# Kernel optimization log

Measured on AMD Instinct MI355X. Metric: run time of the kernel, lower is better.

## Reference

```python
import jax, jax.numpy as jnp
import numpy as np

B, IN, H = 4096, 1024, 2048

def setup_inputs() -> dict:
    key = jax.random.key(0)
    ks = jax.random.split(key, 7)
    sk = (1.0 / H) ** 0.5
    return {
        "x": jax.random.normal(ks[0], (B, IN), dtype=jnp.float32),
        "prev_h": jax.random.normal(ks[1], (B, H), dtype=jnp.float32),
        "prev_c": jax.random.normal(ks[2], (B, H), dtype=jnp.float32),
        "W_i": jax.random.uniform(ks[3], (H, H + IN), dtype=jnp.float32, minval=-sk, maxval=sk),
        "W_f": jax.random.uniform(ks[4], (H, H + IN), dtype=jnp.float32, minval=-sk, maxval=sk),
        "W_o": jax.random.uniform(ks[5], (H, H + IN), dtype=jnp.float32, minval=-sk, maxval=sk),
        "W_c": jax.random.uniform(ks[6], (H, H + IN), dtype=jnp.float32, minval=-sk, maxval=sk),
    }

def reference(x, prev_h, prev_c, W_i, W_f, W_o, W_c):
    # concat (h, x) along features: [B, H+IN]
    hx = jnp.concatenate([prev_h, x], axis=1)
    # stack 4 gate weights -> single GEMM: [B, H+IN] @ [H+IN, 4H]
    W = jnp.concatenate([W_i, W_f, W_o, W_c], axis=0)  # [4H, H+IN]
    gates = hx @ W.T  # [B, 4H]
    gi, gf, go, gc = jnp.split(gates, 4, axis=1)
    i = jax.nn.sigmoid(gi)
    f = jax.nn.sigmoid(gf)
    o = jax.nn.sigmoid(go)
    c_tilde = jnp.tanh(gc)
    next_c = f * prev_c + i * c_tilde
    next_h = o * jnp.tanh(next_c)
    return next_h, next_c
```

## Files before the change

kernel.cpp:

```cpp
#include <hip/hip_runtime.h>
#include <hip/hip_bf16.h>


#define BATCH 4096
#define INW   1024
#define HID   2048
#define GK    3072
#define GN    8192

typedef __attribute__((ext_vector_type(8))) short short8;
typedef __attribute__((ext_vector_type(4))) float floatx4;

__device__ __forceinline__ unsigned short f2bf(float f) {
    union { float f; unsigned u; } v; v.f = f;
    unsigned r = v.u + 0x7FFFu + ((v.u >> 16) & 1u);
    return (unsigned short)(r >> 16);
}
__device__ __forceinline__ float sigf(float x) {
    return 1.0f / (1.0f + __expf(-x));
}
__device__ __forceinline__ float tanhfast(float x) {
    float t = __expf(fminf(fmaxf(2.0f * x, -30.0f), 30.0f));
    return (t - 1.0f) / (t + 1.0f);
}

__global__ __launch_bounds__(256) void pack_all(const float4* __restrict__ ph,
                                                const float4* __restrict__ x,
                                                const float4* __restrict__ Wi,
                                                const float4* __restrict__ Wf,
                                                const float4* __restrict__ Wo,
                                                const float4* __restrict__ Wc,
                                                unsigned short* __restrict__ hx,
                                                unsigned short* __restrict__ Wb) {
    long i = (long)blockIdx.x * 256 + threadIdx.x;
    const float4* src;
    unsigned short* dst;
    if (i < 1048576L) {
        int r  = (int)(i >> 8);
        int c8 = (int)(i & 255);
        src = ph + 2 * i;
        dst = hx + (size_t)r * GK + (size_t)c8 * 8;
    } else if (i < 1572864L) {
        long j = i - 1048576L;
        int r  = (int)(j >> 7);
        int c8 = (int)(j & 127);
        src = x + 2 * j;
        dst = hx + (size_t)r * GK + HID + (size_t)c8 * 8;
    } else {
        long j = i - 1572864L;
        const float4* Wg;
        int g;
        if (j < 786432L)            { Wg = Wi; g = 0; }
        else if (j < 1572864L)      { Wg = Wf; g = 1; j -= 786432L; }
        else if (j < 2359296L)      { Wg = Wo; g = 2; j -= 1572864L; }
        else                        { Wg = Wc; g = 3; j -= 2359296L; }
        src = Wg + 2 * j;
        int h  = (int)(j / 384);
        int kc = (int)(j - (long)h * 384);
        dst = Wb + (size_t)(4 * h + g) * GK + (size_t)kc * 8;
    }
    float4 v0 = src[0];
    float4 v1 = src[1];
    unsigned short o[8];
    o[0] = f2bf(v0.x); o[1] = f2bf(v0.y); o[2] = f2bf(v0.z); o[3] = f2bf(v0.w);
    o[4] = f2bf(v1.x); o[5] = f2bf(v1.y); o[6] = f2bf(v1.z); o[7] = f2bf(v1.w);
    *(short8*)dst = *(const short8*)o;
}

__device__ __forceinline__ void gld16(const unsigned short* g, unsigned short* l) {
    __builtin_amdgcn_global_load_lds((const __attribute__((address_space(1))) unsigned int*)g,
                                     (__attribute__((address_space(3))) unsigned int*)l,
                                     16, 0, 0);
}

template<int VM> __device__ __forceinline__ void wait_vm() {
    if constexpr (VM == 8)      asm volatile("s_waitcnt vmcnt(8)" ::: "memory");
    else if constexpr (VM == 4) asm volatile("s_waitcnt vmcnt(4)" ::: "memory");
    else if constexpr (VM == 0) asm volatile("s_waitcnt vmcnt(0)" ::: "memory");
}

__global__ __launch_bounds__(512, 2) void gemm_fused(const unsigned short* __restrict__ A,
                                                     const unsigned short* __restrict__ Bt,
                                                     const float* __restrict__ prev_c,
                                                     float* __restrict__ out) {
    __shared__ unsigned short lds[65536];
    const int tid  = threadIdx.x;
    const int wave = tid >> 6;
    const int lane = tid & 63;

    const int bid = blockIdx.x;
    const int x = bid & 7, ii = bid >> 3;
    const int mt = ((x & 3) << 2) + (ii & 3);
    const int nt = ((x >> 2) << 4) + (ii >> 2);
    const long row0 = (long)mt * 256;
    const long col0 = (long)nt * 256;

    const int wm = wave >> 2;
    const int wn = wave & 3;

    const int c0 = ((tid & 3) - ((tid >> 3) & 3)) & 3;
    const unsigned short* gA0 = A  + (row0 + (tid >> 2)) * GK + c0 * 8;
    const unsigned short* gB0 = Bt + (col0 + (tid >> 2)) * GK + c0 * 8;

#define STAGE_A(kt, b) do { \
        unsigned short* _d = &lds[(b) * 8192 + tid * 8]; \
        gld16(gA0 + (size_t)(kt) * 32, _d); \
        gld16(gA0 + 128 * GK + (size_t)(kt) * 32, _d + 4096); \
    } while (0)
#define STAGE_B(kt, b) do { \
        unsigned short* _d = &lds[32768 + (b) * 8192 + tid * 8]; \
        gld16(gB0 + (size_t)(kt) * 32, _d); \
        gld16(gB0 + 128 * GK + (size_t)(kt) * 32, _d + 4096); \
    } while (0)

    const int fr = lane & 15;
    const int cq = lane >> 4;
    const int slot = ((cq + (fr >> 1)) & 3) << 3;
    const int aoff = (wm * 128 + fr) * 32 + slot;
    const int boff = (wn * 64 + fr) * 32 + slot;

    floatx4 acc[8][4];
    #pragma unroll
    for (int i = 0; i < 8; i++)
        #pragma unroll
        for (int j = 0; j < 4; j++)
            acc[i][j] = (floatx4)(0.0f);

    STAGE_A(0, 0); STAGE_B(0, 0);
    STAGE_A(1, 1); STAGE_B(1, 1);
    STAGE_A(2, 2); STAGE_B(2, 2);
    asm volatile("s_waitcnt vmcnt(8)" ::: "memory");
    __builtin_amdgcn_s_barrier();

#define K_ITER(t, VMW, STG) do { \
        const unsigned short* bufA = &lds[((t) & 3) * 8192]; \
        const unsigned short* bufB = &lds[32768 + ((t) & 3) * 8192]; \
        short8 af[4], af2[4], bfv[4]; \
        _Pragma("unroll") \
        for (int i = 0; i < 4; i++) af[i]  = *(const short8*)&bufA[aoff + i * 512]; \
        _Pragma("unroll") \
        for (int j = 0; j < 4; j++) bfv[j] = *(const short8*)&bufB[boff + j * 512]; \
        __builtin_amdgcn_sched_barrier(0);  \
        _Pragma("unroll") \
        for (int i = 0; i < 4; i++) af2[i] = *(const short8*)&bufA[aoff + 2048 + i * 512]; \
        if (STG) { STAGE_A((t) + 3, ((t) + 3) & 3); STAGE_B((t) + 3, ((t) + 3) & 3); } \
        asm volatile("s_waitcnt lgkmcnt(4)" ::: "memory"); \
        __builtin_amdgcn_sched_barrier(0); \
        __builtin_amdgcn_s_setprio(1); \
        _Pragma("unroll") \
        for (int i = 0; i < 4; i++) \
            _Pragma("unroll") \
            for (int j = 0; j < 4; j++) \
                acc[i][j] = __builtin_amdgcn_mfma_f32_16x16x32_bf16(af[i], bfv[j], acc[i][j], 0, 0, 0); \
        __builtin_amdgcn_s_setprio(0); \
        asm volatile("s_waitcnt lgkmcnt(0)" ::: "memory"); \
        __builtin_amdgcn_sched_barrier(0); \
        wait_vm<VMW>(); \
        __builtin_amdgcn_s_barrier(); \
        __builtin_amdgcn_sched_barrier(0); \
        __builtin_amdgcn_s_setprio(1); \
        _Pragma("unroll") \
        for (int i = 0; i < 4; i++) \
            _Pragma("unroll") \
            for (int j = 0; j < 4; j++) \
                acc[4 + i][j] = __builtin_amdgcn_mfma_f32_16x16x32_bf16(af2[i], bfv[j], acc[4 + i][j], 0, 0, 0); \
        __builtin_amdgcn_s_setprio(0); \
    } while (0)

    int t = 0;
    for (; t < 93; ++t) K_ITER(t, 8, true);
    K_ITER(93, 4, false);
    K_ITER(94, 0, false);
    K_ITER(95, -1, false);

#undef K_ITER
#undef STAGE_A
#undef STAGE_B

    const int cr = (lane >> 4) << 2;
    const int cc = lane & 15;
    const long hbase = col0 >> 2;
    float* gbuf = (float*)lds;

    #pragma unroll 1
    for (int pass = 0; pass < 2; ++pass) {
        __syncthreads();
        if (wm == pass) {
            #pragma unroll
            for (int mi = 0; mi < 8; mi++) {
                #pragma unroll
                for (int nj = 0; nj < 4; nj++) {
                    const int colb = wn * 64 + nj * 16 + cc;
                    #pragma unroll
                    for (int r = 0; r < 4; r++)
                        gbuf[(mi * 16 + cr + r) * 256 + colb] = acc[mi][nj][r];
                }
            }
        }
        __syncthreads();
        #pragma unroll 4
        for (int p = 0; p < 16; p++) {
            const int u   = p * 512 + tid;
            const int row = u >> 6;
            const int h   = u & 63;
            float4 g4 = *(const float4*)&gbuf[row * 256 + h * 4];
            const long grow = row0 + pass * 128 + row;
            const long ob   = grow * (long)HID + hbase + h;
            float pc = prev_c[ob];
            float iv = sigf(g4.x);
            float fv = sigf(g4.y);
            float ov = sigf(g4.z);
            float cv = tanhfast(g4.w);
            float nc = fv * pc + iv * cv;
            float nh = ov * tanhfast(nc);
            out[ob] = nh;
            out[(size_t)BATCH * HID + ob] = nc;
        }
    }
}

extern "C" void kernel_launch(void* const* d_in, const int* in_sizes, int n_in,
                              void* d_out, int out_size, void* d_ws, size_t ws_size,
                              hipStream_t stream) {
    const float* x   = (const float*)d_in[0];
    const float* ph  = (const float*)d_in[1];
    const float* pc  = (const float*)d_in[2];
    const float* Wi  = (const float*)d_in[3];
    const float* Wf  = (const float*)d_in[4];
    const float* Wo  = (const float*)d_in[5];
    const float* Wc  = (const float*)d_in[6];

    unsigned short* hx = (unsigned short*)d_ws;
    unsigned short* Wb = hx + (size_t)BATCH * GK;
    float* out = (float*)d_out;

    pack_all<<<18432, 256, 0, stream>>>((const float4*)ph, (const float4*)x,
                                        (const float4*)Wi, (const float4*)Wf,
                                        (const float4*)Wo, (const float4*)Wc,
                                        hx, Wb);

    gemm_fused<<<512, 512, 0, stream>>>(hx, Wb, pc, out);
}
```

Baseline: 402.2 us.

## Switch GEMM inner loop to 32x32x16 bf16 MFMA tiles

```diff
diff --git a/kernel.cpp b/kernel.cpp
--- a/kernel.cpp
+++ b/kernel.cpp
@@ -10,6 +10,7 @@
 
 typedef __attribute__((ext_vector_type(8))) short short8;
 typedef __attribute__((ext_vector_type(4))) float floatx4;
+typedef __attribute__((ext_vector_type(16))) float floatx16;
 
 __device__ __forceinline__ unsigned short f2bf(float f) {
     union { float f; unsigned u; } v; v.f = f;
@@ -113,18 +114,23 @@
         gld16(gB0 + 128 * GK + (size_t)(kt) * 32, _d + 4096); \
     } while (0)
 
-    const int fr = lane & 15;
-    const int cq = lane >> 4;
-    const int slot = ((cq + (fr >> 1)) & 3) << 3;
-    const int aoff = (wm * 128 + fr) * 32 + slot;
-    const int boff = (wn * 64 + fr) * 32 + slot;
-
-    floatx4 acc[8][4];
+    const int fr32 = lane & 31;
+    const int hk   = lane >> 5;
+    const int RA0  = wm * 128 + fr32;
+    const int RB0  = wn * 64 + fr32;
+    const int sA   = (RA0 >> 1) & 3;
+    const int sB   = (RB0 >> 1) & 3;
+    const int a_k0 = RA0 * 32 + (((hk)     + sA) & 3) * 8;
+    const int a_k1 = RA0 * 32 + (((2 + hk) + sA) & 3) * 8;
+    const int b_k0 = RB0 * 32 + (((hk)     + sB) & 3) * 8;
+    const int b_k1 = RB0 * 32 + (((2 + hk) + sB) & 3) * 8;
+
+    floatx16 acc[4][2];
     #pragma unroll
-    for (int i = 0; i < 8; i++)
+    for (int i = 0; i < 4; i++)
         #pragma unroll
-        for (int j = 0; j < 4; j++)
-            acc[i][j] = (floatx4)(0.0f);
+        for (int j = 0; j < 2; j++)
+            acc[i][j] = (floatx16)(0.0f);
 
     STAGE_A(0, 0); STAGE_B(0, 0);
     STAGE_A(1, 1); STAGE_B(1, 1);
@@ -135,36 +141,35 @@
 #define K_ITER(t, VMW, STG) do { \
         const unsigned short* bufA = &lds[((t) & 3) * 8192]; \
         const unsigned short* bufB = &lds[32768 + ((t) & 3) * 8192]; \
-        short8 af[4], af2[4], bfv[4]; \
-        _Pragma("unroll") \
-        for (int i = 0; i < 4; i++) af[i]  = *(const short8*)&bufA[aoff + i * 512]; \
-        _Pragma("unroll") \
-        for (int j = 0; j < 4; j++) bfv[j] = *(const short8*)&bufB[boff + j * 512]; \
-        __builtin_amdgcn_sched_barrier(0);  \
-        _Pragma("unroll") \
-        for (int i = 0; i < 4; i++) af2[i] = *(const short8*)&bufA[aoff + 2048 + i * 512]; \
+        short8 af0[4], af1[4], bf0[2], bf1[2]; \
+        _Pragma("unroll") \
+        for (int i = 0; i < 4; i++) { \
+            af0[i] = *(const short8*)&bufA[a_k0 + i * 1024]; \
+            af1[i] = *(const short8*)&bufA[a_k1 + i * 1024]; \
+        } \
+        _Pragma("unroll") \
+        for (int j = 0; j < 2; j++) { \
+            bf0[j] = *(const short8*)&bufB[b_k0 + j * 1024]; \
+            bf1[j] = *(const short8*)&bufB[b_k1 + j * 1024]; \
+        } \
         if (STG) { STAGE_A((t) + 3, ((t) + 3) & 3); STAGE_B((t) + 3, ((t) + 3) & 3); } \
-        asm volatile("s_waitcnt lgkmcnt(4)" ::: "memory"); \
+        __builtin_amdgcn_s_barrier(); \
+        asm volatile("s_waitcnt lgkmcnt(0)" ::: "memory"); \
         __builtin_amdgcn_sched_barrier(0); \
         __builtin_amdgcn_s_setprio(1); \
         _Pragma("unroll") \
         for (int i = 0; i < 4; i++) \
             _Pragma("unroll") \
-            for (int j = 0; j < 4; j++) \
-                acc[i][j] = __builtin_amdgcn_mfma_f32_16x16x32_bf16(af[i], bfv[j], acc[i][j], 0, 0, 0); \
+            for (int j = 0; j < 2; j++) \
+                acc[i][j] = __builtin_amdgcn_mfma_f32_32x32x16_bf16(af0[i], bf0[j], acc[i][j], 0, 0, 0); \
+        _Pragma("unroll") \
+        for (int i = 0; i < 4; i++) \
+            _Pragma("unroll") \
+            for (int j = 0; j < 2; j++) \
+                acc[i][j] = __builtin_amdgcn_mfma_f32_32x32x16_bf16(af1[i], bf1[j], acc[i][j], 0, 0, 0); \
         __builtin_amdgcn_s_setprio(0); \
-        asm volatile("s_waitcnt lgkmcnt(0)" ::: "memory"); \
-        __builtin_amdgcn_sched_barrier(0); \
         wait_vm<VMW>(); \
         __builtin_amdgcn_s_barrier(); \
-        __builtin_amdgcn_sched_barrier(0); \
-        __builtin_amdgcn_s_setprio(1); \
-        _Pragma("unroll") \
-        for (int i = 0; i < 4; i++) \
-            _Pragma("unroll") \
-            for (int j = 0; j < 4; j++) \
-                acc[4 + i][j] = __builtin_amdgcn_mfma_f32_16x16x32_bf16(af2[i], bfv[j], acc[4 + i][j], 0, 0, 0); \
-        __builtin_amdgcn_s_setprio(0); \
     } while (0)
 
     int t = 0;
@@ -177,8 +182,6 @@
 #undef STAGE_A
 #undef STAGE_B
 
-    const int cr = (lane >> 4) << 2;
-    const int cc = lane & 15;
     const long hbase = col0 >> 2;
     float* gbuf = (float*)lds;
 
@@ -187,13 +190,15 @@
         __syncthreads();
         if (wm == pass) {
             #pragma unroll
-            for (int mi = 0; mi < 8; mi++) {
+            for (int mi = 0; mi < 4; mi++) {
                 #pragma unroll
-                for (int nj = 0; nj < 4; nj++) {
-                    const int colb = wn * 64 + nj * 16 + cc;
+                for (int nj = 0; nj < 2; nj++) {
+                    const int colb = wn * 64 + nj * 32 + fr32;
                     #pragma unroll
-                    for (int r = 0; r < 4; r++)
-                        gbuf[(mi * 16 + cr + r) * 256 + colb] = acc[mi][nj][r];
+                    for (int r = 0; r < 16; r++) {
+                        const int row_loc = mi * 32 + (r & 3) + 8 * (r >> 2) + 4 * hk;
+                        gbuf[row_loc * 256 + colb] = acc[mi][nj][r];
+                    }
                 }
             }
         }
```

Result: slower. 437.3 us (+8.7%).

## Split GEMM K-iteration into two phases with register-prefetched next fragments

Applied to the files above, without the earlier changes.

```diff
diff --git a/kernel.cpp b/kernel.cpp
--- a/kernel.cpp
+++ b/kernel.cpp
@@ -73,11 +73,18 @@
                                      16, 0, 0);
 }
 
-template<int VM> __device__ __forceinline__ void wait_vm() {
-    if constexpr (VM == 8)      asm volatile("s_waitcnt vmcnt(8)" ::: "memory");
-    else if constexpr (VM == 4) asm volatile("s_waitcnt vmcnt(4)" ::: "memory");
-    else if constexpr (VM == 0) asm volatile("s_waitcnt vmcnt(0)" ::: "memory");
-}
+template<int N> __device__ __forceinline__ void wait_vm() {
+    if constexpr (N == 8)      asm volatile("s_waitcnt vmcnt(8)" ::: "memory");
+    else if constexpr (N == 6) asm volatile("s_waitcnt vmcnt(6)" ::: "memory");
+    else if constexpr (N == 4) asm volatile("s_waitcnt vmcnt(4)" ::: "memory");
+    else if constexpr (N == 0) asm volatile("s_waitcnt vmcnt(0)" ::: "memory");
+}
+template<int N> __device__ __forceinline__ void wait_lgkm() {
+    if constexpr (N == 8)      asm volatile("s_waitcnt lgkmcnt(8)" ::: "memory");
+    else if constexpr (N == 4) asm volatile("s_waitcnt lgkmcnt(4)" ::: "memory");
+    else if constexpr (N == 0) asm volatile("s_waitcnt lgkmcnt(0)" ::: "memory");
+}
+#define SBAR __builtin_amdgcn_sched_barrier(0)
 
 __global__ __launch_bounds__(512, 2) void gemm_fused(const unsigned short* __restrict__ A,
                                                      const unsigned short* __restrict__ Bt,
@@ -126,54 +133,77 @@
         for (int j = 0; j < 4; j++)
             acc[i][j] = (floatx4)(0.0f);
 
+    short8 afM0[4], afM1[4], bfP[4], bfQ[4];
+
     STAGE_A(0, 0); STAGE_B(0, 0);
     STAGE_A(1, 1); STAGE_B(1, 1);
     STAGE_A(2, 2); STAGE_B(2, 2);
-    asm volatile("s_waitcnt vmcnt(8)" ::: "memory");
+    wait_vm<8>();
     __builtin_amdgcn_s_barrier();
-
-#define K_ITER(t, VMW, STG) do { \
-        const unsigned short* bufA = &lds[((t) & 3) * 8192]; \
-        const unsigned short* bufB = &lds[32768 + ((t) & 3) * 8192]; \
-        short8 af[4], af2[4], bfv[4]; \
+    SBAR;
+    #pragma unroll
+    for (int i = 0; i < 4; i++) afM0[i] = *(const short8*)&lds[aoff + i * 512];
+    #pragma unroll
+    for (int j = 0; j < 4; j++) bfP[j]  = *(const short8*)&lds[32768 + boff + j * 512];
+    SBAR;
+
+#define PH0(T, BCUR, VMW, STG) do { \
+        const unsigned short* bufA = &lds[((T) & 3) * 8192]; \
         _Pragma("unroll") \
-        for (int i = 0; i < 4; i++) af[i]  = *(const short8*)&bufA[aoff + i * 512]; \
-        _Pragma("unroll") \
-        for (int j = 0; j < 4; j++) bfv[j] = *(const short8*)&bufB[boff + j * 512]; \
-        __builtin_amdgcn_sched_barrier(0);  \
-        _Pragma("unroll") \
-        for (int i = 0; i < 4; i++) af2[i] = *(const short8*)&bufA[aoff + 2048 + i * 512]; \
-        if (STG) { STAGE_A((t) + 3, ((t) + 3) & 3); STAGE_B((t) + 3, ((t) + 3) & 3); } \
-        asm volatile("s_waitcnt lgkmcnt(4)" ::: "memory"); \
-        __builtin_amdgcn_sched_barrier(0); \
+        for (int i = 0; i < 4; i++) afM1[i] = *(const short8*)&bufA[aoff + 2048 + i * 512]; \
+        if (STG) { STAGE_A((T) + 3, ((T) + 3) & 3); } \
+        SBAR; \
+        wait_vm<VMW>(); \
+        wait_lgkm<4>(); \
+        SBAR; \
         __builtin_amdgcn_s_setprio(1); \
         _Pragma("unroll") \
         for (int i = 0; i < 4; i++) \
             _Pragma("unroll") \
             for (int j = 0; j < 4; j++) \
-                acc[i][j] = __builtin_amdgcn_mfma_f32_16x16x32_bf16(af[i], bfv[j], acc[i][j], 0, 0, 0); \
+                acc[i][j] = __builtin_amdgcn_mfma_f32_16x16x32_bf16(afM0[i], BCUR[j], acc[i][j], 0, 0, 0); \
         __builtin_amdgcn_s_setprio(0); \
-        asm volatile("s_waitcnt lgkmcnt(0)" ::: "memory"); \
-        __builtin_amdgcn_sched_barrier(0); \
-        wait_vm<VMW>(); \
+        SBAR; \
         __builtin_amdgcn_s_barrier(); \
-        __builtin_amdgcn_sched_barrier(0); \
+        SBAR; \
+    } while (0)
+
+#define PH1(T, BCUR, BNXT, STG, NEXT, LGK) do { \
+        const unsigned short* bufA2 = &lds[(((T) + 1) & 3) * 8192]; \
+        const unsigned short* bufB2 = &lds[32768 + (((T) + 1) & 3) * 8192]; \
+        if (NEXT) { \
+            _Pragma("unroll") \
+            for (int i = 0; i < 4; i++) afM0[i] = *(const short8*)&bufA2[aoff + i * 512]; \
+            _Pragma("unroll") \
+            for (int j = 0; j < 4; j++) BNXT[j] = *(const short8*)&bufB2[boff + j * 512]; \
+        } \
+        if (STG) { STAGE_B((T) + 3, ((T) + 3) & 3); } \
+        SBAR; \
+        wait_lgkm<LGK>(); \
+        SBAR; \
         __builtin_amdgcn_s_setprio(1); \
         _Pragma("unroll") \
         for (int i = 0; i < 4; i++) \
             _Pragma("unroll") \
             for (int j = 0; j < 4; j++) \
-                acc[4 + i][j] = __builtin_amdgcn_mfma_f32_16x16x32_bf16(af2[i], bfv[j], acc[4 + i][j], 0, 0, 0); \
+                acc[4 + i][j] = __builtin_amdgcn_mfma_f32_16x16x32_bf16(afM1[i], BCUR[j], acc[4 + i][j], 0, 0, 0); \
         __builtin_amdgcn_s_setprio(0); \
-    } while (0)
-
-    int t = 0;
-    for (; t < 93; ++t) K_ITER(t, 8, true);
-    K_ITER(93, 4, false);
-    K_ITER(94, 0, false);
-    K_ITER(95, -1, false);
-
-#undef K_ITER
+        SBAR; \
+        __builtin_amdgcn_s_barrier(); \
+        SBAR; \
+    } while (0)
+
+    for (int t = 0; t < 92; t += 2) {
+        PH0(t, bfP, 6, true);      PH1(t, bfP, bfQ, true, true, 8);
+        PH0(t + 1, bfQ, 6, true);  PH1(t + 1, bfQ, bfP, true, true, 8);
+    }
+    PH0(92, bfP, 6, true);   PH1(92, bfP, bfQ, true, true, 8);
+    PH0(93, bfQ, 4, false);  PH1(93, bfQ, bfP, false, true, 8);
+    PH0(94, bfP, 0, false);  PH1(94, bfP, bfQ, false, true, 8);
+    PH0(95, bfQ, 0, false);  PH1(95, bfQ, bfP, false, false, 0);
+
+#undef PH0
+#undef PH1
 #undef STAGE_A
 #undef STAGE_B
 
```

Result: no change. 409.9 us (+1.9%).
